# Optimization experiments

Hardware: AMD Instinct MI355X
Metric: run time of the kernel (lower is better)

Reference implementation:

```python
import jax, jax.numpy as jnp
import numpy as np

B, C, H, W = 8, 256, 128, 128
NUM_S, MIDS, K = 64, 8, 8  # plane_mid, mids, node_num
HW = H * W
EPS = 1e-9


def _pool_mat(n, o):
    # adaptive avg pool 1D as a (o, n) averaging matrix (torch AdaptiveAvgPool2d bins)
    M = np.zeros((o, n), np.float32)
    for i in range(o):
        s = (i * n) // o
        e = -((-(i + 1) * n) // o)  # ceil((i+1)*n/o)
        M[i, s:e] = 1.0 / (e - s)
    return jnp.asarray(M)


def setup_inputs() -> dict:
    key = jax.random.key(0)
    ks = jax.random.split(key, 11)
    rn = lambda k, shp, s=1.0: jax.random.normal(k, shp, jnp.float32) * s
    return {
        "x": rn(ks[0], (B, C, H, W)),
        "contour": rn(ks[1], (B, 2, H, W)),
        "conv_state_w": rn(ks[2], (NUM_S, C), 0.06),
        "conv_state_b": jnp.zeros((NUM_S,), jnp.float32),
        "conv_proj_w": rn(ks[3], (NUM_S, C), 0.06),
        "conv_proj_b": jnp.zeros((NUM_S,), jnp.float32),
        "anchor": jax.random.uniform(ks[4], (K, C), jnp.float32),
        "sigma_p": jax.random.uniform(ks[5], (K, C), jnp.float32),
        "gcn_w1": rn(ks[6], (C, C), 0.06),
        "gcn_w2": rn(ks[7], (C, C), 0.06),
        "gcn_w3": rn(ks[8], (C, C), 0.06),
    }


def reference(x, contour, conv_state_w, conv_state_b, conv_proj_w, conv_proj_b,
              anchor, sigma_p, gcn_w1, gcn_w2, gcn_w3):
    b, c, h, w = x.shape
    hw = h * w
    xf = x.reshape(b, c, hw)                                       # (B,C,HW)

    # ---- EnhanceModule: contour-masked projection -> anchors -> softmax assignment ----
    # contour already at x's spatial size, so F.interpolate is identity
    cm = jax.nn.softmax(contour, axis=1)[:, 1:2]                    # (B,1,H,W)
    x_proj = jnp.einsum('sc,bcn->bsn', conv_proj_w, xf) + conv_proj_b[None, :, None]  # (B,S,HW)
    x_mask = x_proj.reshape(b, NUM_S, h, w) * cm                    # (B,S,H,W)
    Mh, Mw = _pool_mat(h, MIDS + 2), _pool_mat(w, MIDS + 2)
    pooled = jnp.einsum('oh,bshw,pw->bsop', Mh, x_mask, Mw)         # adaptive avg pool (B,S,10,10)
    x_anchor = pooled[:, :, 1:-1, 1:-1].reshape(b, NUM_S, MIDS * MIDS)  # (B,S,mids^2)
    proj = jnp.einsum('bsm,bsn->bmn', x_anchor, x_proj)             # (B,mids^2,HW)
    proj = jax.nn.softmax(proj, axis=1)

    # ---- GraphNet (NetVLAD-style), vectorized over nodes ----
    sigma = jax.nn.sigmoid(sigma_p)                                 # (K,C)
    inv2 = 1.0 / (sigma * sigma)
    xn = xf.transpose(0, 2, 1)                                      # (B,HW,C)
    # ||(x_n - a_k)/sigma_k||^2 via quadratic expansion (no (B,K,HW,C) tensor)
    d2 = (jnp.einsum('bnc,kc->bkn', xn * xn, inv2)
          - 2.0 * jnp.einsum('bnc,kc->bkn', xn, anchor * inv2)
          + jnp.sum(anchor * anchor * inv2, axis=1)[None, :, None])  # (B,K,HW)
    soft = jax.nn.softmax(-0.5 * d2, axis=1)                        # (B,K,HW)
    ssum = soft.sum(-1)                                             # (B,K)
    wsum = jnp.einsum('bkn,bnc->bkc', soft, xn)                     # (B,K,C)
    nodes = (wsum - anchor[None] * ssum[..., None]) / sigma[None] / (ssum[..., None] + EPS)
    nodes = nodes / jnp.maximum(jnp.linalg.norm(nodes, axis=2, keepdims=True), 1e-12)
    flat = nodes.reshape(b, -1)
    flat = flat / jnp.maximum(jnp.linalg.norm(flat, axis=1, keepdims=True), 1e-12)
    g = flat.reshape(b, c, K)  # torch .view reinterpret (NOT transpose)

    # ---- CascadeGCNet, loop=3 ----
    for Wg in (gcn_w1, gcn_w2, gcn_w3):
        gt = g.transpose(0, 2, 1)                                   # (B,K,C)
        adj = jax.nn.softmax(jnp.einsum('bkc,bcj->bkj', gt, g), axis=2)  # (B,K,K)
        support = jnp.einsum('bkc,cd->bkd', gt, Wg)                 # (B,K,C)
        g = jnp.einsum('bkj,bjd->bdk', adj, support)                # (B,C,K)
    g = jax.nn.relu(g)
    return (g, proj, soft)
```

## Files before the change

### kernel.cpp

```cpp
#include <hip/hip_runtime.h>
#include <math.h>

#define HW 16384
#define B_ 8
#define C_ 256
#define S_ 64
#define K_ 8

__device__ __forceinline__ float sigmoidf_(float z) { return 1.f / (1.f + __expf(-z)); }

__global__ __launch_bounds__(256) void k0_prep(const float* __restrict__ anchor,
                                               const float* __restrict__ sigma_p,
                                               const float* __restrict__ wproj,
                                               float* __restrict__ Wt, float* __restrict__ iva2,
                                               float* __restrict__ kconst, float* __restrict__ ssumg) {
    const int c = threadIdx.x;
    const int lane = c & 63, wid = c >> 6;
    __shared__ float red[4][8];
    float kc[8];
#pragma unroll
    for (int k = 0; k < 8; ++k) {
        float sg = sigmoidf_(sigma_p[k * C_ + c]);
        float iv = 1.f / (sg * sg);
        float a = anchor[k * C_ + c];
        const int r = k >> 1, j = k & 1;
        iva2[c * 16 + r * 4 + j] = a * iv;
        iva2[c * 16 + r * 4 + 2 + j] = iv;
        kc[k] = a * a * iv;
    }
    for (int s = 0; s < S_; ++s) Wt[c * S_ + s] = wproj[s * C_ + c];
    if (c < 64) ssumg[c] = 0.f;
#pragma unroll
    for (int m = 32; m; m >>= 1) {
#pragma unroll
        for (int k = 0; k < 8; ++k) kc[k] += __shfl_xor(kc[k], m, 64);
    }
    if (lane == 0) {
#pragma unroll
        for (int k = 0; k < 8; ++k) red[wid][k] = kc[k];
    }
    __syncthreads();
    if (c < 8) kconst[c] = red[0][c] + red[1][c] + red[2][c] + red[3][c];
}

__global__ __launch_bounds__(256) void k1_fused(
    const float* __restrict__ x, const float* __restrict__ contour,
    const float* __restrict__ Wt, const float* __restrict__ bproj,
    const float* __restrict__ iva2, const float* __restrict__ kconst,
    float* __restrict__ cm, float* __restrict__ xp, float* __restrict__ soft,
    float* __restrict__ ssumg) {
    __shared__ float Wl[C_ * S_];
    __shared__ float xl[2][4][256];
    const int tid = threadIdx.x;
    const int lane = tid & 63;
    const int r = __builtin_amdgcn_readfirstlane(tid >> 6);
    const int s0 = r * 16;
    const int b = blockIdx.y;
    const int pxblk = blockIdx.x * 256;
    const int pl = lane * 4;
    const int px = pxblk + pl;

    {
        const float4* src = (const float4*)Wt;
        float4* dst = (float4*)Wl;
        for (int i = tid; i < C_ * S_ / 4; i += 256) dst[i] = src[i];
    }
    {
        const float4 v = *(const float4*)(x + ((size_t)b * C_ + r) * HW + px);
        *(float4*)&xl[0][r][pl] = v;
    }
    __syncthreads();

    float4 acc[16];
#pragma unroll
    for (int s = 0; s < 16; ++s) acc[s] = make_float4(0.f, 0.f, 0.f, 0.f);
    float4 q1a = make_float4(0.f, 0.f, 0.f, 0.f), q1b = q1a, q2a = q1a, q2b = q1a;

    int buf = 0;
    for (int ch = 0; ch < C_; ch += 4) {
        const bool more = (ch + 4) < C_;
        float4 nv;
        if (more) nv = *(const float4*)(x + ((size_t)b * C_ + ch + 4 + r) * HW + px);

#pragma unroll
        for (int j = 0; j < 4; ++j) {
            const int c = ch + j;
            const float4 xv = *(const float4*)&xl[buf][j][pl];
            const float4* wr4 = (const float4*)&Wl[c * S_ + s0];
            const float4 w0 = wr4[0], w1 = wr4[1], w2 = wr4[2], w3 = wr4[3];
#define FMA4(W, S)                                      \
            acc[S].x = fmaf(W, xv.x, acc[S].x);         \
            acc[S].y = fmaf(W, xv.y, acc[S].y);         \
            acc[S].z = fmaf(W, xv.z, acc[S].z);         \
            acc[S].w = fmaf(W, xv.w, acc[S].w);
            FMA4(w0.x, 0)  FMA4(w0.y, 1)  FMA4(w0.z, 2)  FMA4(w0.w, 3)
            FMA4(w1.x, 4)  FMA4(w1.y, 5)  FMA4(w1.z, 6)  FMA4(w1.w, 7)
            FMA4(w2.x, 8)  FMA4(w2.y, 9)  FMA4(w2.z, 10) FMA4(w2.w, 11)
            FMA4(w3.x, 12) FMA4(w3.y, 13) FMA4(w3.z, 14) FMA4(w3.w, 15)
#undef FMA4
            const float4 t = *(const float4*)&iva2[c * 16 + r * 4];
            float4 x2;
            x2.x = xv.x * xv.x; x2.y = xv.y * xv.y; x2.z = xv.z * xv.z; x2.w = xv.w * xv.w;
            q1a.x = fmaf(t.x, xv.x, q1a.x); q1a.y = fmaf(t.x, xv.y, q1a.y);
            q1a.z = fmaf(t.x, xv.z, q1a.z); q1a.w = fmaf(t.x, xv.w, q1a.w);
            q1b.x = fmaf(t.y, xv.x, q1b.x); q1b.y = fmaf(t.y, xv.y, q1b.y);
            q1b.z = fmaf(t.y, xv.z, q1b.z); q1b.w = fmaf(t.y, xv.w, q1b.w);
            q2a.x = fmaf(t.z, x2.x, q2a.x); q2a.y = fmaf(t.z, x2.y, q2a.y);
            q2a.z = fmaf(t.z, x2.z, q2a.z); q2a.w = fmaf(t.z, x2.w, q2a.w);
            q2b.x = fmaf(t.w, x2.x, q2b.x); q2b.y = fmaf(t.w, x2.y, q2b.y);
            q2b.z = fmaf(t.w, x2.z, q2b.z); q2b.w = fmaf(t.w, x2.w, q2b.w);
        }
        if (more) *(float4*)&xl[buf ^ 1][r][pl] = nv;
        __syncthreads();
        buf ^= 1;
    }

#pragma unroll
    for (int s = 0; s < 16; ++s) {
        const float bias = bproj[s0 + s];
        float4 o;
        o.x = acc[s].x + bias; o.y = acc[s].y + bias;
        o.z = acc[s].z + bias; o.w = acc[s].w + bias;
        *(float4*)(xp + ((size_t)b * S_ + s0 + s) * HW + px) = o;
    }

    float* qb = Wl;
    *(float4*)&qb[(2 * r) * 256 + pl] = q1a;
    *(float4*)&qb[(2 * r + 1) * 256 + pl] = q1b;
    *(float4*)&qb[2048 + (2 * r) * 256 + pl] = q2a;
    *(float4*)&qb[2048 + (2 * r + 1) * 256 + pl] = q2b;
    __syncthreads();

    if (r == 0) {
        float4 lgv[K_];
        float4 mx = make_float4(-1e30f, -1e30f, -1e30f, -1e30f);
#pragma unroll
        for (int k = 0; k < K_; ++k) {
            const float4 q1k = *(const float4*)&qb[k * 256 + pl];
            const float4 q2k = *(const float4*)&qb[2048 + k * 256 + pl];
            const float kc = kconst[k];
            lgv[k].x = -0.5f * (q2k.x - 2.f * q1k.x + kc);
            lgv[k].y = -0.5f * (q2k.y - 2.f * q1k.y + kc);
            lgv[k].z = -0.5f * (q2k.z - 2.f * q1k.z + kc);
            lgv[k].w = -0.5f * (q2k.w - 2.f * q1k.w + kc);
            mx.x = fmaxf(mx.x, lgv[k].x); mx.y = fmaxf(mx.y, lgv[k].y);
            mx.z = fmaxf(mx.z, lgv[k].z); mx.w = fmaxf(mx.w, lgv[k].w);
        }
        float4 sm = make_float4(0.f, 0.f, 0.f, 0.f);
#pragma unroll
        for (int k = 0; k < K_; ++k) {
            lgv[k].x = __expf(lgv[k].x - mx.x); sm.x += lgv[k].x;
            lgv[k].y = __expf(lgv[k].y - mx.y); sm.y += lgv[k].y;
            lgv[k].z = __expf(lgv[k].z - mx.z); sm.z += lgv[k].z;
            lgv[k].w = __expf(lgv[k].w - mx.w); sm.w += lgv[k].w;
        }
        const float ix = 1.f / sm.x, iy = 1.f / sm.y, iz = 1.f / sm.z, iw = 1.f / sm.w;
        float ssk[K_];
#pragma unroll
        for (int k = 0; k < K_; ++k) {
            float4 o;
            o.x = lgv[k].x * ix; o.y = lgv[k].y * iy;
            o.z = lgv[k].z * iz; o.w = lgv[k].w * iw;
            *(float4*)(soft + ((size_t)b * K_ + k) * HW + px) = o;
            ssk[k] = (o.x + o.y) + (o.z + o.w);
        }
#pragma unroll
        for (int m = 32; m; m >>= 1) {
#pragma unroll
            for (int k = 0; k < K_; ++k) ssk[k] += __shfl_xor(ssk[k], m, 64);
        }
        if (lane == 0) {
#pragma unroll
            for (int k = 0; k < K_; ++k) atomicAdd(ssumg + b * 8 + k, ssk[k]);
        }

        const float4 c0 = *(const float4*)(contour + (size_t)b * 2 * HW + px);
        const float4 c1 = *(const float4*)(contour + (size_t)b * 2 * HW + HW + px);
        float4 cv;
        cv.x = sigmoidf_(c1.x - c0.x); cv.y = sigmoidf_(c1.y - c0.y);
        cv.z = sigmoidf_(c1.z - c0.z); cv.w = sigmoidf_(c1.w - c0.w);
        *(float4*)(cm + (size_t)b * HW + px) = cv;
    }
}

__global__ void k2_anchor(const float* __restrict__ xp, const float* __restrict__ cm,
                          float* __restrict__ xa) {
    __shared__ float col[128];
    const int i = blockIdx.x;
    const int s = blockIdx.y;
    const int b = blockIdx.z;
    const int w = threadIdx.x;
    const int h0 = ((i + 1) * 128) / 10;
    const int h1 = ((i + 2) * 128 + 9) / 10;
    const float* xps = xp + ((size_t)b * S_ + s) * HW;
    const float* cmb = cm + (size_t)b * HW;
    float v = 0.f;
    for (int h = h0; h < h1; ++h) v += xps[h * 128 + w] * cmb[h * 128 + w];
    col[w] = v;
    __syncthreads();
    if (w < 8) {
        const int j = w;
        const int w0 = ((j + 1) * 128) / 10;
        const int w1 = ((j + 2) * 128 + 9) / 10;
        float sum = 0.f;
        for (int t = w0; t < w1; ++t) sum += col[t];
        xa[((size_t)b * S_ + s) * 64 + i * 8 + j] = sum / (float)((h1 - h0) * (w1 - w0));
    }
}

__global__ __launch_bounds__(256, 4) void k3_proj(const float* __restrict__ xa,
                                                  float* __restrict__ xp) {
    const int tid = threadIdx.x;
    const int lane = tid & 63;
    const int wid = __builtin_amdgcn_readfirstlane(tid >> 6);
    const int pg = wid & 1;
    const int sh = wid >> 1;
    const int b = blockIdx.y;
    const int n = blockIdx.x * 128 + pg * 64 + lane;
    const float* xab = xa + (size_t)b * 4096;

    float p[64];
#pragma unroll
    for (int m = 0; m < 64; ++m) p[m] = 0.f;

    float* xpb = xp + (size_t)b * S_ * HW + n;
    const int s0 = sh * 32;
    float xv = xpb[(size_t)s0 * HW];
    for (int si = 0; si < 32; ++si) {
        const int s = s0 + si;
        float xnext = (si < 31) ? xpb[(size_t)(s + 1) * HW] : 0.f;
        const float* row = xab + s * 64;
#pragma unroll
        for (int m = 0; m < 64; ++m) p[m] = fmaf(row[m], xv, p[m]);
        xv = xnext;
    }

    __shared__ float lds[2][64][64];
    if (sh) {
#pragma unroll
        for (int m = 0; m < 64; ++m) lds[pg][m][lane] = p[m];
    }
    __syncthreads();
    if (!sh) {
#pragma unroll
        for (int m = 0; m < 64; ++m) p[m] += lds[pg][m][lane];
        float mx = -1e30f;
#pragma unroll
        for (int m = 0; m < 64; ++m) mx = fmaxf(mx, p[m]);
        float sm = 0.f;
#pragma unroll
        for (int m = 0; m < 64; ++m) { float e = __expf(p[m] - mx); p[m] = e; sm += e; }
        const float inv = 1.f / sm;
#pragma unroll
        for (int m = 0; m < 64; ++m) xpb[(size_t)m * HW] = p[m] * inv;
    }
}

__global__ __launch_bounds__(256) void k5_wsum(const float* __restrict__ x,
                                               const float* __restrict__ soft,
                                               float* __restrict__ wsum) {
    const int b = blockIdx.y;
    const int c0 = blockIdx.x * 2;
    const int tid = threadIdx.x;
    float a[16];
#pragma unroll
    for (int i = 0; i < 16; ++i) a[i] = 0.f;
    const float4* sb = (const float4*)(soft + (size_t)b * K_ * HW);
    const float4* xb = (const float4*)(x + ((size_t)b * C_ + c0) * HW);
    for (int i = tid; i < HW / 4; i += 256) {
        float4 sv[8];
#pragma unroll
        for (int k = 0; k < 8; ++k) sv[k] = sb[(size_t)k * (HW / 4) + i];
#pragma unroll
        for (int ci = 0; ci < 2; ++ci) {
            float4 xv = xb[(size_t)ci * (HW / 4) + i];
#pragma unroll
            for (int k = 0; k < 8; ++k) {
                float t = fmaf(sv[k].x, xv.x, fmaf(sv[k].y, xv.y,
                          fmaf(sv[k].z, xv.z, sv[k].w * xv.w)));
                a[ci * 8 + k] += t;
            }
        }
    }
    __shared__ float red[64];
    const int lane = tid & 63, wid = tid >> 6;
#pragma unroll
    for (int o = 0; o < 16; ++o) {
        float v = a[o];
#pragma unroll
        for (int m = 32; m; m >>= 1) v += __shfl_xor(v, m, 64);
        if (lane == 0) red[wid * 16 + o] = v;
    }
    __syncthreads();
    if (tid < 16) {
        float r = red[tid] + red[16 + tid] + red[32 + tid] + red[48 + tid];
        int ci = tid >> 3, k = tid & 7;
        wsum[((size_t)b * K_ + k) * C_ + c0 + ci] = r;
    }
}

__device__ __forceinline__ float blockSum256(float v, volatile float* sc) {
#pragma unroll
    for (int m = 32; m; m >>= 1) v += __shfl_xor(v, m, 64);
    const int wid = threadIdx.x >> 6, lane = threadIdx.x & 63;
    __syncthreads();
    if (lane == 0) sc[wid] = v;
    __syncthreads();
    return sc[0] + sc[1] + sc[2] + sc[3];
}

__global__ __launch_bounds__(256) void k6_gcn(const float* __restrict__ ssumg,
                                              const float* __restrict__ wsum,
                                              const float* __restrict__ anchor,
                                              const float* __restrict__ sigma_p,
                                              const float* __restrict__ w1,
                                              const float* __restrict__ w2,
                                              const float* __restrict__ w3,
                                              float* __restrict__ gout) {
    const int b = blockIdx.x;
    const int tid = threadIdx.x;
    const int lane = tid & 63, wid = tid >> 6;
    __shared__ float g_lds[2048];
    __shared__ float A[64];
    __shared__ float sc[4];
    __shared__ float red8[4][8];
    __shared__ float ssk_s[8];

    if (tid < 8) ssk_s[tid] = ssumg[b * 8 + tid];
    __syncthreads();
    float ssk[8];
#pragma unroll
    for (int k = 0; k < 8; ++k) ssk[k] = ssk_s[k];

    const int c = tid;
    float node[8];
#pragma unroll
    for (int k = 0; k < 8; ++k) {
        float sg = sigmoidf_(sigma_p[k * C_ + c]);
        float w = wsum[((size_t)b * K_ + k) * C_ + c];
        node[k] = (w - anchor[k * C_ + c] * ssk[k]) / sg / (ssk[k] + 1e-9f);
    }
    float rn[8];
#pragma unroll
    for (int k = 0; k < 8; ++k) rn[k] = node[k] * node[k];
#pragma unroll
    for (int m = 32; m; m >>= 1) {
#pragma unroll
        for (int k = 0; k < 8; ++k) rn[k] += __shfl_xor(rn[k], m, 64);
    }
    if (lane == 0) {
#pragma unroll
        for (int k = 0; k < 8; ++k) red8[wid][k] = rn[k];
    }
    __syncthreads();
#pragma unroll
    for (int k = 0; k < 8; ++k) {
        float t = red8[0][k] + red8[1][k] + red8[2][k] + red8[3][k];
        node[k] /= fmaxf(sqrtf(t), 1e-12f);
    }
    float fs = 0.f;
#pragma unroll
    for (int k = 0; k < 8; ++k) fs += node[k] * node[k];
    float fn = blockSum256(fs, sc);
    float finv = 1.f / fmaxf(sqrtf(fn), 1e-12f);
#pragma unroll
    for (int k = 0; k < 8; ++k) g_lds[tid * 8 + k] = node[k] * finv;
    __syncthreads();

    const float* Ws[3] = {w1, w2, w3};
    for (int L = 0; L < 3; ++L) {
        {
            const int pair = tid >> 2, part = tid & 3;
            const int p = pair >> 3, q = pair & 7;
            float s = 0.f;
            for (int i = part * 64; i < part * 64 + 64; ++i)
                s += g_lds[i * 8 + p] * g_lds[i * 8 + q];
            s += __shfl_xor(s, 1, 64);
            s += __shfl_xor(s, 2, 64);
            if (part == 0) A[pair] = s;
        }
        __syncthreads();
        if (tid < 8) {
            float mx = -1e30f;
            for (int j = 0; j < 8; ++j) mx = fmaxf(mx, A[tid * 8 + j]);
            float sm = 0.f;
            for (int j = 0; j < 8; ++j) { float e = __expf(A[tid * 8 + j] - mx); A[tid * 8 + j] = e; sm += e; }
            float iv = 1.f / sm;
            for (int j = 0; j < 8; ++j) A[tid * 8 + j] *= iv;
        }
        __syncthreads();
        float sup[8];
#pragma unroll
        for (int j = 0; j < 8; ++j) sup[j] = 0.f;
        const float* W = Ws[L];
        float wv[8], wn[8];
#pragma unroll
        for (int i = 0; i < 8; ++i) wv[i] = W[(size_t)i * 256 + tid];
        for (int c0 = 0; c0 < 256; c0 += 8) {
            if (c0 + 8 < 256) {
#pragma unroll
                for (int i = 0; i < 8; ++i) wn[i] = W[(size_t)(c0 + 8 + i) * 256 + tid];
            }
#pragma unroll
            for (int i = 0; i < 8; ++i) {
#pragma unroll
                for (int j = 0; j < 8; ++j)
                    sup[j] = fmaf(g_lds[(c0 + i) * 8 + j], wv[i], sup[j]);
            }
#pragma unroll
            for (int i = 0; i < 8; ++i) wv[i] = wn[i];
        }
        float gn[8];
#pragma unroll
        for (int k = 0; k < 8; ++k) {
            float s = 0.f;
#pragma unroll
            for (int j = 0; j < 8; ++j) s += A[k * 8 + j] * sup[j];
            gn[k] = s;
        }
        __syncthreads();
#pragma unroll
        for (int k = 0; k < 8; ++k) g_lds[tid * 8 + k] = gn[k];
        __syncthreads();
    }
#pragma unroll
    for (int k = 0; k < 8; ++k)
        gout[(size_t)b * 2048 + tid * 8 + k] = fmaxf(g_lds[tid * 8 + k], 0.f);
}

extern "C" void kernel_launch(void* const* d_in, const int* in_sizes, int n_in,
                              void* d_out, int out_size, void* d_ws, size_t ws_size,
                              hipStream_t stream) {
    const float* x = (const float*)d_in[0];
    const float* contour = (const float*)d_in[1];
    const float* wproj = (const float*)d_in[4];
    const float* bproj = (const float*)d_in[5];
    const float* anchor = (const float*)d_in[6];
    const float* sigma_p = (const float*)d_in[7];
    const float* w1 = (const float*)d_in[8];
    const float* w2 = (const float*)d_in[9];
    const float* w3 = (const float*)d_in[10];

    float* out = (float*)d_out;
    float* g_out = out;
    float* xp = out + 16384;
    float* soft = out + 16384 + 8388608;

    float* ws = (float*)d_ws;
    float* cm = ws;
    float* xa = ws + 131072;
    float* wsum = ws + 163840;
    float* kconst = ws + 180224;
    float* ssumg = ws + 180232;
    float* Wt = ws + 180296;
    float* iva2 = ws + 196680;

    k0_prep<<<1, 256, 0, stream>>>(anchor, sigma_p, wproj, Wt, iva2, kconst, ssumg);
    k1_fused<<<dim3(HW / 256, B_), 256, 0, stream>>>(x, contour, Wt, bproj, iva2, kconst,
                                                     cm, xp, soft, ssumg);
    k2_anchor<<<dim3(8, 64, B_), 128, 0, stream>>>(xp, cm, xa);
    k3_proj<<<dim3(HW / 128, B_), 256, 0, stream>>>(xa, xp);
    k5_wsum<<<dim3(128, B_), 256, 0, stream>>>(x, soft, wsum);
    k6_gcn<<<B_, 256, 0, stream>>>(ssumg, wsum, anchor, sigma_p, w1, w2, w3, g_out);
}
```

Measured before the change: 240.2 us.

## Replace LDS-staged x double buffer with per-wave register prefetch ring

Each wave now loads x channels directly from global memory into a rotating set of four registers, prefetching four channels ahead, instead of cooperatively staging x in shared memory. This removes a block-wide barrier and LDS round trip every four channels. iva2 is also copied into shared memory once rather than read from global memory inside the loop. In exchange, all four waves redundantly load the same x rows, raising cache and L2 traffic, and register pressure grows.

```diff
diff --git a/kernel.cpp b/kernel.cpp
--- a/kernel.cpp
+++ b/kernel.cpp
@@ -50,24 +50,22 @@
     float* __restrict__ cm, float* __restrict__ xp, float* __restrict__ soft,
     float* __restrict__ ssumg) {
     __shared__ float Wl[C_ * S_];
-    __shared__ float xl[2][4][256];
+    __shared__ float Ql[C_ * 16];
     const int tid = threadIdx.x;
     const int lane = tid & 63;
     const int r = __builtin_amdgcn_readfirstlane(tid >> 6);
     const int s0 = r * 16;
     const int b = blockIdx.y;
-    const int pxblk = blockIdx.x * 256;
     const int pl = lane * 4;
-    const int px = pxblk + pl;
+    const int px = blockIdx.x * 256 + pl;
 
     {
         const float4* src = (const float4*)Wt;
         float4* dst = (float4*)Wl;
         for (int i = tid; i < C_ * S_ / 4; i += 256) dst[i] = src[i];
-    }
-    {
-        const float4 v = *(const float4*)(x + ((size_t)b * C_ + r) * HW + px);
-        *(float4*)&xl[0][r][pl] = v;
+        const float4* qs = (const float4*)iva2;
+        float4* qd = (float4*)Ql;
+        for (int i = tid; i < C_ * 16 / 4; i += 256) qd[i] = qs[i];
     }
     __syncthreads();
 
@@ -76,44 +74,70 @@
     for (int s = 0; s < 16; ++s) acc[s] = make_float4(0.f, 0.f, 0.f, 0.f);
     float4 q1a = make_float4(0.f, 0.f, 0.f, 0.f), q1b = q1a, q2a = q1a, q2b = q1a;
 
-    int buf = 0;
-    for (int ch = 0; ch < C_; ch += 4) {
-        const bool more = (ch + 4) < C_;
-        float4 nv;
-        if (more) nv = *(const float4*)(x + ((size_t)b * C_ + ch + 4 + r) * HW + px);
-
-#pragma unroll
-        for (int j = 0; j < 4; ++j) {
-            const int c = ch + j;
-            const float4 xv = *(const float4*)&xl[buf][j][pl];
-            const float4* wr4 = (const float4*)&Wl[c * S_ + s0];
-            const float4 w0 = wr4[0], w1 = wr4[1], w2 = wr4[2], w3 = wr4[3];
-#define FMA4(W, S)                                      \
-            acc[S].x = fmaf(W, xv.x, acc[S].x);         \
-            acc[S].y = fmaf(W, xv.y, acc[S].y);         \
-            acc[S].z = fmaf(W, xv.z, acc[S].z);         \
-            acc[S].w = fmaf(W, xv.w, acc[S].w);
-            FMA4(w0.x, 0)  FMA4(w0.y, 1)  FMA4(w0.z, 2)  FMA4(w0.w, 3)
-            FMA4(w1.x, 4)  FMA4(w1.y, 5)  FMA4(w1.z, 6)  FMA4(w1.w, 7)
-            FMA4(w2.x, 8)  FMA4(w2.y, 9)  FMA4(w2.z, 10) FMA4(w2.w, 11)
-            FMA4(w3.x, 12) FMA4(w3.y, 13) FMA4(w3.z, 14) FMA4(w3.w, 15)
-#undef FMA4
-            const float4 t = *(const float4*)&iva2[c * 16 + r * 4];
-            float4 x2;
-            x2.x = xv.x * xv.x; x2.y = xv.y * xv.y; x2.z = xv.z * xv.z; x2.w = xv.w * xv.w;
-            q1a.x = fmaf(t.x, xv.x, q1a.x); q1a.y = fmaf(t.x, xv.y, q1a.y);
-            q1a.z = fmaf(t.x, xv.z, q1a.z); q1a.w = fmaf(t.x, xv.w, q1a.w);
-            q1b.x = fmaf(t.y, xv.x, q1b.x); q1b.y = fmaf(t.y, xv.y, q1b.y);
-            q1b.z = fmaf(t.y, xv.z, q1b.z); q1b.w = fmaf(t.y, xv.w, q1b.w);
-            q2a.x = fmaf(t.z, x2.x, q2a.x); q2a.y = fmaf(t.z, x2.y, q2a.y);
-            q2a.z = fmaf(t.z, x2.z, q2a.z); q2a.w = fmaf(t.z, x2.w, q2a.w);
-            q2b.x = fmaf(t.w, x2.x, q2b.x); q2b.y = fmaf(t.w, x2.y, q2b.y);
-            q2b.z = fmaf(t.w, x2.z, q2b.z); q2b.w = fmaf(t.w, x2.w, q2b.w);
-        }
-        if (more) *(float4*)&xl[buf ^ 1][r][pl] = nv;
-        __syncthreads();
-        buf ^= 1;
-    }
+    const float* xb = x + (size_t)b * C_ * HW + px;
+    float4 a0 = *(const float4*)(xb);
+    float4 a1 = *(const float4*)(xb + (size_t)1 * HW);
+    float4 a2 = *(const float4*)(xb + (size_t)2 * HW);
+    float4 a3 = *(const float4*)(xb + (size_t)3 * HW);
+
+#define BODY(REG, CC, CN)                                                          \
+    {                                                                              \
+        const float4 xv = REG;                                                     \
+        if ((CN) < C_) REG = *(const float4*)(xb + (size_t)(CN) * HW);             \
+        const float4* wr4 = (const float4*)&Wl[(CC) * S_ + s0];                    \
+        const float4 w0 = wr4[0], w1 = wr4[1], w2 = wr4[2], w3 = wr4[3];           \
+        const float4 t = *(const float4*)&Ql[(CC) * 16 + r * 4];                   \
+        acc[0].x = fmaf(w0.x, xv.x, acc[0].x);  acc[0].y = fmaf(w0.x, xv.y, acc[0].y);   \
+        acc[0].z = fmaf(w0.x, xv.z, acc[0].z);  acc[0].w = fmaf(w0.x, xv.w, acc[0].w);   \
+        acc[1].x = fmaf(w0.y, xv.x, acc[1].x);  acc[1].y = fmaf(w0.y, xv.y, acc[1].y);   \
+        acc[1].z = fmaf(w0.y, xv.z, acc[1].z);  acc[1].w = fmaf(w0.y, xv.w, acc[1].w);   \
+        acc[2].x = fmaf(w0.z, xv.x, acc[2].x);  acc[2].y = fmaf(w0.z, xv.y, acc[2].y);   \
+        acc[2].z = fmaf(w0.z, xv.z, acc[2].z);  acc[2].w = fmaf(w0.z, xv.w, acc[2].w);   \
+        acc[3].x = fmaf(w0.w, xv.x, acc[3].x);  acc[3].y = fmaf(w0.w, xv.y, acc[3].y);   \
+        acc[3].z = fmaf(w0.w, xv.z, acc[3].z);  acc[3].w = fmaf(w0.w, xv.w, acc[3].w);   \
+        acc[4].x = fmaf(w1.x, xv.x, acc[4].x);  acc[4].y = fmaf(w1.x, xv.y, acc[4].y);   \
+        acc[4].z = fmaf(w1.x, xv.z, acc[4].z);  acc[4].w = fmaf(w1.x, xv.w, acc[4].w);   \
+        acc[5].x = fmaf(w1.y, xv.x, acc[5].x);  acc[5].y = fmaf(w1.y, xv.y, acc[5].y);   \
+        acc[5].z = fmaf(w1.y, xv.z, acc[5].z);  acc[5].w = fmaf(w1.y, xv.w, acc[5].w);   \
+        acc[6].x = fmaf(w1.z, xv.x, acc[6].x);  acc[6].y = fmaf(w1.z, xv.y, acc[6].y);   \
+        acc[6].z = fmaf(w1.z, xv.z, acc[6].z);  acc[6].w = fmaf(w1.z, xv.w, acc[6].w);   \
+        acc[7].x = fmaf(w1.w, xv.x, acc[7].x);  acc[7].y = fmaf(w1.w, xv.y, acc[7].y);   \
+        acc[7].z = fmaf(w1.w, xv.z, acc[7].z);  acc[7].w = fmaf(w1.w, xv.w, acc[7].w);   \
+        acc[8].x = fmaf(w2.x, xv.x, acc[8].x);  acc[8].y = fmaf(w2.x, xv.y, acc[8].y);   \
+        acc[8].z = fmaf(w2.x, xv.z, acc[8].z);  acc[8].w = fmaf(w2.x, xv.w, acc[8].w);   \
+        acc[9].x = fmaf(w2.y, xv.x, acc[9].x);  acc[9].y = fmaf(w2.y, xv.y, acc[9].y);   \
+        acc[9].z = fmaf(w2.y, xv.z, acc[9].z);  acc[9].w = fmaf(w2.y, xv.w, acc[9].w);   \
+        acc[10].x = fmaf(w2.z, xv.x, acc[10].x); acc[10].y = fmaf(w2.z, xv.y, acc[10].y); \
+        acc[10].z = fmaf(w2.z, xv.z, acc[10].z); acc[10].w = fmaf(w2.z, xv.w, acc[10].w); \
+        acc[11].x = fmaf(w2.w, xv.x, acc[11].x); acc[11].y = fmaf(w2.w, xv.y, acc[11].y); \
+        acc[11].z = fmaf(w2.w, xv.z, acc[11].z); acc[11].w = fmaf(w2.w, xv.w, acc[11].w); \
+        acc[12].x = fmaf(w3.x, xv.x, acc[12].x); acc[12].y = fmaf(w3.x, xv.y, acc[12].y); \
+        acc[12].z = fmaf(w3.x, xv.z, acc[12].z); acc[12].w = fmaf(w3.x, xv.w, acc[12].w); \
+        acc[13].x = fmaf(w3.y, xv.x, acc[13].x); acc[13].y = fmaf(w3.y, xv.y, acc[13].y); \
+        acc[13].z = fmaf(w3.y, xv.z, acc[13].z); acc[13].w = fmaf(w3.y, xv.w, acc[13].w); \
+        acc[14].x = fmaf(w3.z, xv.x, acc[14].x); acc[14].y = fmaf(w3.z, xv.y, acc[14].y); \
+        acc[14].z = fmaf(w3.z, xv.z, acc[14].z); acc[14].w = fmaf(w3.z, xv.w, acc[14].w); \
+        acc[15].x = fmaf(w3.w, xv.x, acc[15].x); acc[15].y = fmaf(w3.w, xv.y, acc[15].y); \
+        acc[15].z = fmaf(w3.w, xv.z, acc[15].z); acc[15].w = fmaf(w3.w, xv.w, acc[15].w); \
+        float4 x2;                                                                 \
+        x2.x = xv.x * xv.x; x2.y = xv.y * xv.y; x2.z = xv.z * xv.z; x2.w = xv.w * xv.w; \
+        q1a.x = fmaf(t.x, xv.x, q1a.x); q1a.y = fmaf(t.x, xv.y, q1a.y);            \
+        q1a.z = fmaf(t.x, xv.z, q1a.z); q1a.w = fmaf(t.x, xv.w, q1a.w);            \
+        q1b.x = fmaf(t.y, xv.x, q1b.x); q1b.y = fmaf(t.y, xv.y, q1b.y);            \
+        q1b.z = fmaf(t.y, xv.z, q1b.z); q1b.w = fmaf(t.y, xv.w, q1b.w);            \
+        q2a.x = fmaf(t.z, x2.x, q2a.x); q2a.y = fmaf(t.z, x2.y, q2a.y);            \
+        q2a.z = fmaf(t.z, x2.z, q2a.z); q2a.w = fmaf(t.z, x2.w, q2a.w);            \
+        q2b.x = fmaf(t.w, x2.x, q2b.x); q2b.y = fmaf(t.w, x2.y, q2b.y);            \
+        q2b.z = fmaf(t.w, x2.z, q2b.z); q2b.w = fmaf(t.w, x2.w, q2b.w);            \
+    }
+
+    for (int c = 0; c < C_; c += 4) {
+        BODY(a0, c + 0, c + 4)
+        BODY(a1, c + 1, c + 5)
+        BODY(a2, c + 2, c + 6)
+        BODY(a3, c + 3, c + 7)
+    }
+#undef BODY
 
 #pragma unroll
     for (int s = 0; s < 16; ++s) {
@@ -124,6 +148,7 @@
         *(float4*)(xp + ((size_t)b * S_ + s0 + s) * HW + px) = o;
     }
 
+    __syncthreads();
     float* qb = Wl;
     *(float4*)&qb[(2 * r) * 256 + pl] = q1a;
     *(float4*)&qb[(2 * r + 1) * 256 + pl] = q1b;
```

New measurement: 250.4 us. 1.04x slower.
